# Optimization experiments

Hardware: AMD Instinct MI355X
Metric: run time of the kernel (lower is better)

Reference implementation:

```python
import jax, jax.numpy as jnp
import numpy as np

N = 50000
E = 800000
IN_C = 256
HID = 256
OUT_C = 128


def _glorot(key, fan_in, fan_out):
    lim = float(np.sqrt(6.0 / (fan_in + fan_out)))
    return jax.random.uniform(key, (fan_in, fan_out), jnp.float32, -lim, lim)


def setup_inputs() -> dict:
    key = jax.random.key(0)
    ks = jax.random.split(key, 10)
    x = jax.random.normal(ks[0], (N, IN_C), dtype=jnp.float32)
    edge_index = jax.random.randint(ks[1], (2, E), 0, N, dtype=jnp.int64)
    return {
        "x": x,
        "edge_index": edge_index,
        # layer 0 MLP: Linear(IN_C,HID)+ReLU+Linear(HID,HID)+ReLU
        "eps0": jnp.zeros((), jnp.float32),
        "W1_0": _glorot(ks[2], IN_C, HID),
        "b1_0": jnp.zeros((HID,), jnp.float32),
        "W2_0": _glorot(ks[3], HID, HID),
        "b2_0": jnp.zeros((HID,), jnp.float32),
        # layer 1 MLP: Linear(HID,HID)+ReLU+Linear(HID,OUT_C)
        "eps1": jnp.zeros((), jnp.float32),
        "W1_1": _glorot(ks[4], HID, HID),
        "b1_1": jnp.zeros((HID,), jnp.float32),
        "W2_1": _glorot(ks[5], HID, OUT_C),
        "b2_1": jnp.zeros((OUT_C,), jnp.float32),
    }


def _gin_layer(x, src, dst, eps, W1, b1, W2, b2, final_relu):
    # sum-aggregate messages x[src] into dst nodes
    agg = jax.ops.segment_sum(x[src], dst, num_segments=N)  # [N, d]
    h = (1.0 + eps) * x + agg
    h = jax.nn.relu(h @ W1 + b1)
    h = h @ W2 + b2
    return jax.nn.relu(h) if final_relu else h


def reference(x, edge_index, eps0, W1_0, b1_0, W2_0, b2_0, eps1, W1_1, b1_1, W2_1, b2_1):
    src, dst = edge_index[0], edge_index[1]
    h = _gin_layer(x, src, dst, eps0, W1_0, b1_0, W2_0, b2_0, final_relu=True)
    h = jax.nn.relu(h)  # model-level ReLU between layers
    h = _gin_layer(h, src, dst, eps1, W1_1, b1_1, W2_1, b2_1, final_relu=False)
    return jax.nn.log_softmax(h, axis=1)
```

## Files before the change

### kernel.cpp

```cpp
#include <hip/hip_runtime.h>
#include <hip/hip_bf16.h>

#define FDIM 256
#define OUTC 128
#define CAP  96

typedef float floatx4 __attribute__((ext_vector_type(4)));
typedef float floatx2 __attribute__((ext_vector_type(2)));
typedef __bf16 bf16x8 __attribute__((ext_vector_type(8)));

__device__ __forceinline__ unsigned short f2bf(float f) {
    union { float f; unsigned u; } v; v.f = f;
    unsigned r = v.u + 0x7FFF + ((v.u >> 16) & 1);
    return (unsigned short)(r >> 16);
}
__device__ __forceinline__ unsigned pack2(float a, float b) {
    return ((unsigned)f2bf(a)) | (((unsigned)f2bf(b)) << 16);
}
__device__ __forceinline__ void acc_row2(floatx2* a, uint4 v) {
    union { unsigned u; float f; } lo, hi;
    lo.u = v.x << 16; hi.u = v.x & 0xffff0000u; a[0] += (floatx2){lo.f, hi.f};
    lo.u = v.y << 16; hi.u = v.y & 0xffff0000u; a[1] += (floatx2){lo.f, hi.f};
    lo.u = v.z << 16; hi.u = v.z & 0xffff0000u; a[2] += (floatx2){lo.f, hi.f};
    lo.u = v.w << 16; hi.u = v.w & 0xffff0000u; a[3] += (floatx2){lo.f, hi.f};
}

__global__ __launch_bounds__(256)
void prep_kernel(const int* __restrict__ src, const int* __restrict__ dst,
                 int* __restrict__ cursor, int* __restrict__ esrc2, int E,
                 const float* __restrict__ x, unsigned short* __restrict__ xb, int total8,
                 const float* __restrict__ W1_0, const float* __restrict__ W2_0,
                 const float* __restrict__ W1_1, const float* __restrict__ W2_1,
                 unsigned short* __restrict__ w1f_0, unsigned short* __restrict__ w2f_0,
                 unsigned short* __restrict__ w1f_1, unsigned short* __restrict__ w2f_1) {
    int gid = blockIdx.x * 256 + threadIdx.x;
    if (gid < E) {
        int d = dst[gid];
        int pos = atomicAdd(&cursor[d], 1);
        if (pos < CAP) esrc2[d * CAP + pos] = src[gid];
        return;
    }
    gid -= E;
    if (gid < total8) {
        const float4* p = (const float4*)(x + (size_t)gid * 8);
        float4 a = p[0], b = p[1];
        uint4 o;
        o.x = pack2(a.x, a.y); o.y = pack2(a.z, a.w);
        o.z = pack2(b.x, b.y); o.w = pack2(b.z, b.w);
        *(uint4*)(xb + (size_t)gid * 8) = o;
        return;
    }
    gid -= total8;
    const int S = FDIM * FDIM;
    const float* W; unsigned short* WF; int local, J, Ncols;
    if (gid < S)          { W = W1_0; WF = w1f_0; local = gid;         J = 4; Ncols = FDIM; }
    else if (gid < 2 * S) { W = W2_0; WF = w2f_0; local = gid - S;     J = 4; Ncols = FDIM; }
    else if (gid < 3 * S) { W = W1_1; WF = w1f_1; local = gid - 2 * S; J = 4; Ncols = FDIM; }
    else if (gid < 3 * S + FDIM * OUTC)
                          { W = W2_1; WF = w2f_1; local = gid - 3 * S; J = 2; Ncols = OUTC; }
    else return;
    int e    = local & 7;
    int lane = (local >> 3) & 63;
    int l15  = lane & 15;
    int quad = lane >> 4;
    int rest = local >> 9;
    int j  = rest % J;  rest /= J;
    int kc = rest & 7;
    int g  = rest >> 3;
    int n = g * (16 * J) + j * 16 + l15;
    int k = kc * 32 + quad * 8 + e;
    WF[local] = f2bf(W[(size_t)k * Ncols + n]);
}

template<bool SELF_F32>
__global__ __launch_bounds__(256)
void gather2_kernel(const unsigned short* __restrict__ xb,
                    const float* __restrict__ xf,
                    const int* __restrict__ esrc2,
                    const int* __restrict__ cursor,
                    const float* __restrict__ epsp, unsigned short* __restrict__ out,
                    int N) {
    int node = (int)((blockIdx.x * blockDim.x + threadIdx.x) >> 6);
    int lane = threadIdx.x & 63;
    if (node >= N) return;
    int half = lane >> 5;
    int hl   = lane & 31;
    int beg = node * CAP;
    int cnt = cursor[node];
    if (cnt > CAP) cnt = CAP;

    floatx2 acc[4];
    acc[0] = (floatx2){0.f, 0.f}; acc[1] = (floatx2){0.f, 0.f};
    acc[2] = (floatx2){0.f, 0.f}; acc[3] = (floatx2){0.f, 0.f};

    int e = 0;
    for (; e + 16 <= cnt; e += 16) {
        int s[8];
        #pragma unroll
        for (int k = 0; k < 8; ++k) s[k] = esrc2[beg + e + 2 * k + half];
        uint4 v[8];
        #pragma unroll
        for (int k = 0; k < 8; ++k)
            v[k] = *(const uint4*)(xb + (size_t)s[k] * FDIM + hl * 8);
        #pragma unroll
        for (int k = 0; k < 8; ++k) acc_row2(acc, v[k]);
    }
    for (; e + 4 <= cnt; e += 4) {
        int s0 = esrc2[beg + e + half];
        int s1 = esrc2[beg + e + 2 + half];
        uint4 v0 = *(const uint4*)(xb + (size_t)s0 * FDIM + hl * 8);
        uint4 v1 = *(const uint4*)(xb + (size_t)s1 * FDIM + hl * 8);
        acc_row2(acc, v0);
        acc_row2(acc, v1);
    }
    if (e + 2 <= cnt) {
        int s0 = esrc2[beg + e + half];
        uint4 v0 = *(const uint4*)(xb + (size_t)s0 * FDIM + hl * 8);
        acc_row2(acc, v0);
        e += 2;
    }
    if (e < cnt && half == 0) {
        int s0 = esrc2[beg + e];
        uint4 v0 = *(const uint4*)(xb + (size_t)s0 * FDIM + hl * 8);
        acc_row2(acc, v0);
    }

    float a8[8];
    #pragma unroll
    for (int i = 0; i < 4; ++i) { a8[2 * i] = acc[i][0]; a8[2 * i + 1] = acc[i][1]; }
    #pragma unroll
    for (int i = 0; i < 8; ++i) a8[i] += __shfl_xor(a8[i], 32);

    if (half == 0) {
        float scale = 1.0f + *epsp;
        if (SELF_F32) {
            const float4* p = (const float4*)(xf + (size_t)node * FDIM + hl * 8);
            float4 a = p[0], b = p[1];
            a8[0] += scale * a.x; a8[1] += scale * a.y;
            a8[2] += scale * a.z; a8[3] += scale * a.w;
            a8[4] += scale * b.x; a8[5] += scale * b.y;
            a8[6] += scale * b.z; a8[7] += scale * b.w;
        } else {
            uint4 v = *(const uint4*)(xb + (size_t)node * FDIM + hl * 8);
            union { unsigned u; float f; } t;
            t.u = v.x << 16;         a8[0] += scale * t.f;
            t.u = v.x & 0xffff0000u; a8[1] += scale * t.f;
            t.u = v.y << 16;         a8[2] += scale * t.f;
            t.u = v.y & 0xffff0000u; a8[3] += scale * t.f;
            t.u = v.z << 16;         a8[4] += scale * t.f;
            t.u = v.z & 0xffff0000u; a8[5] += scale * t.f;
            t.u = v.w << 16;         a8[6] += scale * t.f;
            t.u = v.w & 0xffff0000u; a8[7] += scale * t.f;
        }
        uint4 o;
        o.x = pack2(a8[0], a8[1]);
        o.y = pack2(a8[2], a8[3]);
        o.z = pack2(a8[4], a8[5]);
        o.w = pack2(a8[6], a8[7]);
        *(uint4*)(out + (size_t)node * FDIM + hl * 8) = o;
    }
}

#define LDA 264

template<bool FINAL>
__global__ __launch_bounds__(256)
void mlp_fused_kernel(const unsigned short* __restrict__ A,
                      const unsigned short* __restrict__ W1F,
                      const float* __restrict__ b1,
                      const unsigned short* __restrict__ W2F,
                      const float* __restrict__ b2,
                      void* __restrict__ Out, int M) {
    __shared__ unsigned short As[64 * LDA];
    __shared__ float sred[64 * 4 * 2];

    int tid  = threadIdx.x;
    int wave = tid >> 6;
    int lane = tid & 63;
    int l15  = lane & 15;
    int quad = lane >> 4;
    int row0 = blockIdx.x * 64;

    #pragma unroll
    for (int i = 0; i < 8; ++i) {
        int idx = i * 256 + tid;
        int r = idx >> 5;
        int c = (idx & 31) * 8;
        uint4 v = make_uint4(0u, 0u, 0u, 0u);
        int gr = row0 + r;
        if (gr < M) v = *(const uint4*)(A + (size_t)gr * FDIM + c);
        *(uint4*)(As + r * LDA + c) = v;
    }
    __syncthreads();

    floatx4 zero = {0.f, 0.f, 0.f, 0.f};

    {
        floatx4 acc[4][4];
        #pragma unroll
        for (int i = 0; i < 4; ++i)
            #pragma unroll
            for (int j = 0; j < 4; ++j) acc[i][j] = zero;

        const unsigned short* Wb = W1F + (size_t)wave * 16384;
        bf16x8 bcur[4], bnxt[4];
        #pragma unroll
        for (int j = 0; j < 4; ++j)
            bcur[j] = *(const bf16x8*)(Wb + j * 512 + lane * 8);

        for (int kc = 0; kc < 8; ++kc) {
            const unsigned short* Wn = Wb + ((kc < 7) ? (kc + 1) : kc) * 2048;
            #pragma unroll
            for (int j = 0; j < 4; ++j)
                bnxt[j] = *(const bf16x8*)(Wn + j * 512 + lane * 8);
            bf16x8 af[4];
            int k = kc * 32;
            #pragma unroll
            for (int i = 0; i < 4; ++i)
                af[i] = *(const bf16x8*)(As + (i * 16 + l15) * LDA + k + quad * 8);
            #pragma unroll
            for (int i = 0; i < 4; ++i)
                #pragma unroll
                for (int j = 0; j < 4; ++j)
                    acc[i][j] = __builtin_amdgcn_mfma_f32_16x16x32_bf16(
                        af[i], bcur[j], acc[i][j], 0, 0, 0);
            #pragma unroll
            for (int j = 0; j < 4; ++j) bcur[j] = bnxt[j];
        }

        __syncthreads();

        #pragma unroll
        for (int j = 0; j < 4; ++j) {
            int col = wave * 64 + j * 16 + l15;
            float bv = b1[col];
            #pragma unroll
            for (int i = 0; i < 4; ++i) {
                #pragma unroll
                for (int r = 0; r < 4; ++r) {
                    float v = fmaxf(acc[i][j][r] + bv, 0.f);
                    As[(i * 16 + quad * 4 + r) * LDA + col] = f2bf(v);
                }
            }
        }
    }
    __syncthreads();

    if (!FINAL) {
        floatx4 acc[4][4];
        #pragma unroll
        for (int i = 0; i < 4; ++i)
            #pragma unroll
            for (int j = 0; j < 4; ++j) acc[i][j] = zero;

        const unsigned short* Wb = W2F + (size_t)wave * 16384;
        bf16x8 bcur[4], bnxt[4];
        #pragma unroll
        for (int j = 0; j < 4; ++j)
            bcur[j] = *(const bf16x8*)(Wb + j * 512 + lane * 8);

        for (int kc = 0; kc < 8; ++kc) {
            const unsigned short* Wn = Wb + ((kc < 7) ? (kc + 1) : kc) * 2048;
            #pragma unroll
            for (int j = 0; j < 4; ++j)
                bnxt[j] = *(const bf16x8*)(Wn + j * 512 + lane * 8);
            bf16x8 af[4];
            int k = kc * 32;
            #pragma unroll
            for (int i = 0; i < 4; ++i)
                af[i] = *(const bf16x8*)(As + (i * 16 + l15) * LDA + k + quad * 8);
            #pragma unroll
            for (int i = 0; i < 4; ++i)
                #pragma unroll
                for (int j = 0; j < 4; ++j)
                    acc[i][j] = __builtin_amdgcn_mfma_f32_16x16x32_bf16(
                        af[i], bcur[j], acc[i][j], 0, 0, 0);
            #pragma unroll
            for (int j = 0; j < 4; ++j) bcur[j] = bnxt[j];
        }

        unsigned short* O = (unsigned short*)Out;
        #pragma unroll
        for (int j = 0; j < 4; ++j) {
            int col = wave * 64 + j * 16 + l15;
            float bv = b2[col];
            #pragma unroll
            for (int i = 0; i < 4; ++i) {
                #pragma unroll
                for (int r = 0; r < 4; ++r) {
                    int grow = row0 + i * 16 + quad * 4 + r;
                    if (grow < M) {
                        float v = fmaxf(acc[i][j][r] + bv, 0.f);
                        O[(size_t)grow * FDIM + col] = f2bf(v);
                    }
                }
            }
        }
    } else {
        floatx4 acc[4][2];
        #pragma unroll
        for (int i = 0; i < 4; ++i)
            #pragma unroll
            for (int j = 0; j < 2; ++j) acc[i][j] = zero;

        const unsigned short* Wb = W2F + (size_t)wave * 8192;
        bf16x8 bcur[2], bnxt[2];
        #pragma unroll
        for (int j = 0; j < 2; ++j)
            bcur[j] = *(const bf16x8*)(Wb + j * 512 + lane * 8);

        for (int kc = 0; kc < 8; ++kc) {
            const unsigned short* Wn = Wb + ((kc < 7) ? (kc + 1) : kc) * 1024;
            #pragma unroll
            for (int j = 0; j < 2; ++j)
                bnxt[j] = *(const bf16x8*)(Wn + j * 512 + lane * 8);
            bf16x8 af[4];
            int k = kc * 32;
            #pragma unroll
            for (int i = 0; i < 4; ++i)
                af[i] = *(const bf16x8*)(As + (i * 16 + l15) * LDA + k + quad * 8);
            #pragma unroll
            for (int i = 0; i < 4; ++i)
                #pragma unroll
                for (int j = 0; j < 2; ++j)
                    acc[i][j] = __builtin_amdgcn_mfma_f32_16x16x32_bf16(
                        af[i], bcur[j], acc[i][j], 0, 0, 0);
            #pragma unroll
            for (int j = 0; j < 2; ++j) bcur[j] = bnxt[j];
        }

        #pragma unroll
        for (int j = 0; j < 2; ++j) {
            float bv = b2[wave * 32 + j * 16 + l15];
            #pragma unroll
            for (int i = 0; i < 4; ++i)
                #pragma unroll
                for (int r = 0; r < 4; ++r) acc[i][j][r] += bv;
        }

        float* smax = sred;
        float* ssum = sred + 256;

        #pragma unroll
        for (int i = 0; i < 4; ++i) {
            #pragma unroll
            for (int r = 0; r < 4; ++r) {
                float m = fmaxf(acc[i][0][r], acc[i][1][r]);
                #pragma unroll
                for (int off = 1; off < 16; off <<= 1) m = fmaxf(m, __shfl_xor(m, off));
                int row = i * 16 + quad * 4 + r;
                if (l15 == 0) smax[row * 4 + wave] = m;
            }
        }
        __syncthreads();

        float Mloc[4][4];
        #pragma unroll
        for (int i = 0; i < 4; ++i) {
            #pragma unroll
            for (int r = 0; r < 4; ++r) {
                int row = i * 16 + quad * 4 + r;
                float Mr = fmaxf(fmaxf(smax[row * 4 + 0], smax[row * 4 + 1]),
                                 fmaxf(smax[row * 4 + 2], smax[row * 4 + 3]));
                Mloc[i][r] = Mr;
                float s = __expf(acc[i][0][r] - Mr) + __expf(acc[i][1][r] - Mr);
                #pragma unroll
                for (int off = 1; off < 16; off <<= 1) s += __shfl_xor(s, off);
                if (l15 == 0) ssum[row * 4 + wave] = s;
            }
        }
        __syncthreads();

        float* O = (float*)Out;
        #pragma unroll
        for (int i = 0; i < 4; ++i) {
            #pragma unroll
            for (int r = 0; r < 4; ++r) {
                int row = i * 16 + quad * 4 + r;
                int grow = row0 + row;
                if (grow < M) {
                    float lse = Mloc[i][r] +
                        __logf(ssum[row * 4 + 0] + ssum[row * 4 + 1] +
                               ssum[row * 4 + 2] + ssum[row * 4 + 3]);
                    #pragma unroll
                    for (int j = 0; j < 2; ++j) {
                        int col = wave * 32 + j * 16 + l15;
                        O[(size_t)grow * OUTC + col] = acc[i][j][r] - lse;
                    }
                }
            }
        }
    }
}

extern "C" void kernel_launch(void* const* d_in, const int* in_sizes, int n_in,
                              void* d_out, int out_size, void* d_ws, size_t ws_size,
                              hipStream_t stream) {
    const float* x    = (const float*)d_in[0];
    const int*   ei   = (const int*)d_in[1];
    const float* eps0 = (const float*)d_in[2];
    const float* W1_0 = (const float*)d_in[3];
    const float* b1_0 = (const float*)d_in[4];
    const float* W2_0 = (const float*)d_in[5];
    const float* b2_0 = (const float*)d_in[6];
    const float* eps1 = (const float*)d_in[7];
    const float* W1_1 = (const float*)d_in[8];
    const float* b1_1 = (const float*)d_in[9];
    const float* W2_1 = (const float*)d_in[10];
    const float* b2_1 = (const float*)d_in[11];
    float* out = (float*)d_out;

    const int N = in_sizes[0] / FDIM;
    const int E = in_sizes[1] / 2;
    const int* src = ei;
    const int* dst = ei + E;

    size_t buf_elems = (size_t)N * FDIM;
    unsigned short* agg = (unsigned short*)d_ws;
    unsigned short* h2  = agg + buf_elems;
    unsigned short* xb  = h2 + buf_elems;
    unsigned short* w1f_0 = xb + buf_elems;
    unsigned short* w2f_0 = w1f_0 + FDIM * FDIM;
    unsigned short* w1f_1 = w2f_0 + FDIM * FDIM;
    unsigned short* w2f_1 = w1f_1 + FDIM * FDIM;
    int* cursor = (int*)(w2f_1 + FDIM * OUTC);
    int* esrc2  = cursor + N;

    int gather_blocks = (N + 3) / 4;
    int mlp_blocks = (N + 63) / 64;
    int total8 = (int)(buf_elems / 8);
    int wtot = 3 * FDIM * FDIM + FDIM * OUTC;
    int prep_threads = E + total8 + wtot;

    hipMemsetAsync(cursor, 0, (size_t)N * sizeof(int), stream);
    prep_kernel<<<(prep_threads + 255) / 256, 256, 0, stream>>>(
        src, dst, cursor, esrc2, E, x, xb, total8,
        W1_0, W2_0, W1_1, W2_1, w1f_0, w2f_0, w1f_1, w2f_1);

    gather2_kernel<true><<<gather_blocks, 256, 0, stream>>>(
        xb, x, esrc2, cursor, eps0, agg, N);
    mlp_fused_kernel<false><<<mlp_blocks, 256, 0, stream>>>(
        agg, w1f_0, b1_0, w2f_0, b2_0, h2, N);

    gather2_kernel<false><<<gather_blocks, 256, 0, stream>>>(
        h2, nullptr, esrc2, cursor, eps1, agg, N);
    mlp_fused_kernel<true><<<mlp_blocks, 256, 0, stream>>>(
        agg, w1f_1, b1_1, w2f_1, b2_1, out, N);
}
```

Baseline: 349.8 us.

## Fuse neighbor gather-aggregation into the MLP kernel via shared-memory staging

Replaces the separate gather kernel and MLP kernel with one kernel per layer. Each block's waves aggregate their 16 nodes' neighbor rows directly into shared memory before the fused two-layer GEMM. This removes the intermediate aggregated buffer's global write and read and two launches. A zero row is appended so partially filled edge chunks read padding instead of branching. The risk is reduced memory-level parallelism for the irregular gather, since fewer waves, bounded by LDS use, now do serial per-node gathers.

```diff
diff --git a/kernel.cpp b/kernel.cpp
--- a/kernel.cpp
+++ b/kernel.cpp
@@ -1,9 +1,9 @@
 #include <hip/hip_runtime.h>
-#include <hip/hip_bf16.h>
 
 #define FDIM 256
 #define OUTC 128
 #define CAP  96
+#define LDA 264
 
 typedef float floatx4 __attribute__((ext_vector_type(4)));
 typedef float floatx2 __attribute__((ext_vector_type(2)));
@@ -32,7 +32,8 @@
                  const float* __restrict__ W1_0, const float* __restrict__ W2_0,
                  const float* __restrict__ W1_1, const float* __restrict__ W2_1,
                  unsigned short* __restrict__ w1f_0, unsigned short* __restrict__ w2f_0,
-                 unsigned short* __restrict__ w1f_1, unsigned short* __restrict__ w2f_1) {
+                 unsigned short* __restrict__ w1f_1, unsigned short* __restrict__ w2f_1,
+                 unsigned short* __restrict__ xzrow, unsigned short* __restrict__ hzrow) {
     int gid = blockIdx.x * 256 + threadIdx.x;
     if (gid < E) {
         int d = dst[gid];
@@ -52,125 +53,45 @@
     }
     gid -= total8;
     const int S = FDIM * FDIM;
-    const float* W; unsigned short* WF; int local, J, Ncols;
-    if (gid < S)          { W = W1_0; WF = w1f_0; local = gid;         J = 4; Ncols = FDIM; }
-    else if (gid < 2 * S) { W = W2_0; WF = w2f_0; local = gid - S;     J = 4; Ncols = FDIM; }
-    else if (gid < 3 * S) { W = W1_1; WF = w1f_1; local = gid - 2 * S; J = 4; Ncols = FDIM; }
-    else if (gid < 3 * S + FDIM * OUTC)
-                          { W = W2_1; WF = w2f_1; local = gid - 3 * S; J = 2; Ncols = OUTC; }
-    else return;
-    int e    = local & 7;
-    int lane = (local >> 3) & 63;
-    int l15  = lane & 15;
-    int quad = lane >> 4;
-    int rest = local >> 9;
-    int j  = rest % J;  rest /= J;
-    int kc = rest & 7;
-    int g  = rest >> 3;
-    int n = g * (16 * J) + j * 16 + l15;
-    int k = kc * 32 + quad * 8 + e;
-    WF[local] = f2bf(W[(size_t)k * Ncols + n]);
-}
-
-template<bool SELF_F32>
+    const int wtot = 3 * S + FDIM * OUTC;
+    if (gid < wtot) {
+        const float* W; unsigned short* WF; int local, J, Ncols;
+        if (gid < S)          { W = W1_0; WF = w1f_0; local = gid;         J = 4; Ncols = FDIM; }
+        else if (gid < 2 * S) { W = W2_0; WF = w2f_0; local = gid - S;     J = 4; Ncols = FDIM; }
+        else if (gid < 3 * S) { W = W1_1; WF = w1f_1; local = gid - 2 * S; J = 4; Ncols = FDIM; }
+        else                  { W = W2_1; WF = w2f_1; local = gid - 3 * S; J = 2; Ncols = OUTC; }
+        int e    = local & 7;
+        int lane = (local >> 3) & 63;
+        int l15  = lane & 15;
+        int quad = lane >> 4;
+        int rest = local >> 9;
+        int j  = rest % J;  rest /= J;
+        int kc = rest & 7;
+        int g  = rest >> 3;
+        int n = g * (16 * J) + j * 16 + l15;
+        int k = kc * 32 + quad * 8 + e;
+        WF[local] = f2bf(W[(size_t)k * Ncols + n]);
+        return;
+    }
+    gid -= wtot;
+    uint4 z = make_uint4(0u, 0u, 0u, 0u);
+    if (gid < 32) { *(uint4*)(xzrow + gid * 8) = z; return; }
+    gid -= 32;
+    if (gid < 32) { *(uint4*)(hzrow + gid * 8) = z; }
+}
+
+template<bool SELF_F32, bool FINAL>
 __global__ __launch_bounds__(256)
-void gather2_kernel(const unsigned short* __restrict__ xb,
+void gin_mlp_kernel(const unsigned short* __restrict__ xb,
                     const float* __restrict__ xf,
                     const int* __restrict__ esrc2,
                     const int* __restrict__ cursor,
-                    const float* __restrict__ epsp, unsigned short* __restrict__ out,
-                    int N) {
-    int node = (int)((blockIdx.x * blockDim.x + threadIdx.x) >> 6);
-    int lane = threadIdx.x & 63;
-    if (node >= N) return;
-    int half = lane >> 5;
-    int hl   = lane & 31;
-    int beg = node * CAP;
-    int cnt = cursor[node];
-    if (cnt > CAP) cnt = CAP;
-
-    floatx2 acc[4];
-    acc[0] = (floatx2){0.f, 0.f}; acc[1] = (floatx2){0.f, 0.f};
-    acc[2] = (floatx2){0.f, 0.f}; acc[3] = (floatx2){0.f, 0.f};
-
-    int e = 0;
-    for (; e + 16 <= cnt; e += 16) {
-        int s[8];
-        #pragma unroll
-        for (int k = 0; k < 8; ++k) s[k] = esrc2[beg + e + 2 * k + half];
-        uint4 v[8];
-        #pragma unroll
-        for (int k = 0; k < 8; ++k)
-            v[k] = *(const uint4*)(xb + (size_t)s[k] * FDIM + hl * 8);
-        #pragma unroll
-        for (int k = 0; k < 8; ++k) acc_row2(acc, v[k]);
-    }
-    for (; e + 4 <= cnt; e += 4) {
-        int s0 = esrc2[beg + e + half];
-        int s1 = esrc2[beg + e + 2 + half];
-        uint4 v0 = *(const uint4*)(xb + (size_t)s0 * FDIM + hl * 8);
-        uint4 v1 = *(const uint4*)(xb + (size_t)s1 * FDIM + hl * 8);
-        acc_row2(acc, v0);
-        acc_row2(acc, v1);
-    }
-    if (e + 2 <= cnt) {
-        int s0 = esrc2[beg + e + half];
-        uint4 v0 = *(const uint4*)(xb + (size_t)s0 * FDIM + hl * 8);
-        acc_row2(acc, v0);
-        e += 2;
-    }
-    if (e < cnt && half == 0) {
-        int s0 = esrc2[beg + e];
-        uint4 v0 = *(const uint4*)(xb + (size_t)s0 * FDIM + hl * 8);
-        acc_row2(acc, v0);
-    }
-
-    float a8[8];
-    #pragma unroll
-    for (int i = 0; i < 4; ++i) { a8[2 * i] = acc[i][0]; a8[2 * i + 1] = acc[i][1]; }
-    #pragma unroll
-    for (int i = 0; i < 8; ++i) a8[i] += __shfl_xor(a8[i], 32);
-
-    if (half == 0) {
-        float scale = 1.0f + *epsp;
-        if (SELF_F32) {
-            const float4* p = (const float4*)(xf + (size_t)node * FDIM + hl * 8);
-            float4 a = p[0], b = p[1];
-            a8[0] += scale * a.x; a8[1] += scale * a.y;
-            a8[2] += scale * a.z; a8[3] += scale * a.w;
-            a8[4] += scale * b.x; a8[5] += scale * b.y;
-            a8[6] += scale * b.z; a8[7] += scale * b.w;
-        } else {
-            uint4 v = *(const uint4*)(xb + (size_t)node * FDIM + hl * 8);
-            union { unsigned u; float f; } t;
-            t.u = v.x << 16;         a8[0] += scale * t.f;
-            t.u = v.x & 0xffff0000u; a8[1] += scale * t.f;
-            t.u = v.y << 16;         a8[2] += scale * t.f;
-            t.u = v.y & 0xffff0000u; a8[3] += scale * t.f;
-            t.u = v.z << 16;         a8[4] += scale * t.f;
-            t.u = v.z & 0xffff0000u; a8[5] += scale * t.f;
-            t.u = v.w << 16;         a8[6] += scale * t.f;
-            t.u = v.w & 0xffff0000u; a8[7] += scale * t.f;
-        }
-        uint4 o;
-        o.x = pack2(a8[0], a8[1]);
-        o.y = pack2(a8[2], a8[3]);
-        o.z = pack2(a8[4], a8[5]);
-        o.w = pack2(a8[6], a8[7]);
-        *(uint4*)(out + (size_t)node * FDIM + hl * 8) = o;
-    }
-}
-
-#define LDA 264
-
-template<bool FINAL>
-__global__ __launch_bounds__(256)
-void mlp_fused_kernel(const unsigned short* __restrict__ A,
-                      const unsigned short* __restrict__ W1F,
-                      const float* __restrict__ b1,
-                      const unsigned short* __restrict__ W2F,
-                      const float* __restrict__ b2,
-                      void* __restrict__ Out, int M) {
+                    const float* __restrict__ epsp,
+                    const unsigned short* __restrict__ W1F,
+                    const float* __restrict__ b1,
+                    const unsigned short* __restrict__ W2F,
+                    const float* __restrict__ b2,
+                    void* __restrict__ Out, int N) {
     __shared__ unsigned short As[64 * LDA];
     __shared__ float sred[64 * 4 * 2];
 
@@ -179,17 +100,72 @@
     int lane = tid & 63;
     int l15  = lane & 15;
     int quad = lane >> 4;
+    int half = lane >> 5;
+    int hl   = lane & 31;
     int row0 = blockIdx.x * 64;
 
-    #pragma unroll
-    for (int i = 0; i < 8; ++i) {
-        int idx = i * 256 + tid;
-        int r = idx >> 5;
-        int c = (idx & 31) * 8;
-        uint4 v = make_uint4(0u, 0u, 0u, 0u);
-        int gr = row0 + r;
-        if (gr < M) v = *(const uint4*)(A + (size_t)gr * FDIM + c);
-        *(uint4*)(As + r * LDA + c) = v;
+    float scale = 1.0f + *epsp;
+
+    for (int i = 0; i < 16; ++i) {
+        int lrow = wave * 16 + i;
+        int node = row0 + lrow;
+        floatx2 acc[4];
+        acc[0] = (floatx2){0.f, 0.f}; acc[1] = (floatx2){0.f, 0.f};
+        acc[2] = (floatx2){0.f, 0.f}; acc[3] = (floatx2){0.f, 0.f};
+        bool valid = node < N;
+        int cnt = 0;
+        if (valid) { cnt = cursor[node]; if (cnt > CAP) cnt = CAP; }
+        int beg = node * CAP;
+        for (int e = 0; e < cnt; e += 16) {
+            int s[8];
+            #pragma unroll
+            for (int k = 0; k < 8; ++k) {
+                int slot = e + 2 * k + half;
+                int si = esrc2[beg + slot];
+                s[k] = (slot < cnt) ? si : N;
+            }
+            uint4 v[8];
+            #pragma unroll
+            for (int k = 0; k < 8; ++k)
+                v[k] = *(const uint4*)(xb + (size_t)s[k] * FDIM + hl * 8);
+            #pragma unroll
+            for (int k = 0; k < 8; ++k) acc_row2(acc, v[k]);
+        }
+        float a8[8];
+        #pragma unroll
+        for (int j = 0; j < 4; ++j) { a8[2 * j] = acc[j][0]; a8[2 * j + 1] = acc[j][1]; }
+        #pragma unroll
+        for (int j = 0; j < 8; ++j) a8[j] += __shfl_xor(a8[j], 32);
+
+        if (half == 0) {
+            if (valid) {
+                if (SELF_F32) {
+                    const float4* p = (const float4*)(xf + (size_t)node * FDIM + hl * 8);
+                    float4 a = p[0], b = p[1];
+                    a8[0] += scale * a.x; a8[1] += scale * a.y;
+                    a8[2] += scale * a.z; a8[3] += scale * a.w;
+                    a8[4] += scale * b.x; a8[5] += scale * b.y;
+                    a8[6] += scale * b.z; a8[7] += scale * b.w;
+                } else {
+                    uint4 v = *(const uint4*)(xb + (size_t)node * FDIM + hl * 8);
+                    union { unsigned u; float f; } t;
+                    t.u = v.x << 16;         a8[0] += scale * t.f;
+                    t.u = v.x & 0xffff0000u; a8[1] += scale * t.f;
+                    t.u = v.y << 16;         a8[2] += scale * t.f;
+                    t.u = v.y & 0xffff0000u; a8[3] += scale * t.f;
+                    t.u = v.z << 16;         a8[4] += scale * t.f;
+                    t.u = v.z & 0xffff0000u; a8[5] += scale * t.f;
+                    t.u = v.w << 16;         a8[6] += scale * t.f;
+                    t.u = v.w & 0xffff0000u; a8[7] += scale * t.f;
+                }
+            }
+            uint4 o;
+            o.x = pack2(a8[0], a8[1]);
+            o.y = pack2(a8[2], a8[3]);
+            o.z = pack2(a8[4], a8[5]);
+            o.w = pack2(a8[6], a8[7]);
+            *(uint4*)(As + lrow * LDA + hl * 8) = o;
+        }
     }
     __syncthreads();
 
@@ -289,7 +265,7 @@
                 #pragma unroll
                 for (int r = 0; r < 4; ++r) {
                     int grow = row0 + i * 16 + quad * 4 + r;
-                    if (grow < M) {
+                    if (grow < N) {
                         float v = fmaxf(acc[i][j][r] + bv, 0.f);
                         O[(size_t)grow * FDIM + col] = f2bf(v);
                     }
@@ -378,7 +354,7 @@
             for (int r = 0; r < 4; ++r) {
                 int row = i * 16 + quad * 4 + r;
                 int grow = row0 + row;
-                if (grow < M) {
+                if (grow < N) {
                     float lse = Mloc[i][r] +
                         __logf(ssum[row * 4 + 0] + ssum[row * 4 + 1] +
                                ssum[row * 4 + 2] + ssum[row * 4 + 3]);
@@ -415,35 +391,30 @@
     const int* src = ei;
     const int* dst = ei + E;
 
-    size_t buf_elems = (size_t)N * FDIM;
-    unsigned short* agg = (unsigned short*)d_ws;
-    unsigned short* h2  = agg + buf_elems;
-    unsigned short* xb  = h2 + buf_elems;
-    unsigned short* w1f_0 = xb + buf_elems;
+    size_t row_elems = (size_t)(N + 1) * FDIM;
+    unsigned short* h2  = (unsigned short*)d_ws;
+    unsigned short* xb  = h2 + row_elems;
+    unsigned short* w1f_0 = xb + row_elems;
     unsigned short* w2f_0 = w1f_0 + FDIM * FDIM;
     unsigned short* w1f_1 = w2f_0 + FDIM * FDIM;
     unsigned short* w2f_1 = w1f_1 + FDIM * FDIM;
     int* cursor = (int*)(w2f_1 + FDIM * OUTC);
     int* esrc2  = cursor + N;
 
-    int gather_blocks = (N + 3) / 4;
     int mlp_blocks = (N + 63) / 64;
-    int total8 = (int)(buf_elems / 8);
+    int total8 = (int)((size_t)N * FDIM / 8);
     int wtot = 3 * FDIM * FDIM + FDIM * OUTC;
-    int prep_threads = E + total8 + wtot;
+    int prep_threads = E + total8 + wtot + 64;
 
     hipMemsetAsync(cursor, 0, (size_t)N * sizeof(int), stream);
     prep_kernel<<<(prep_threads + 255) / 256, 256, 0, stream>>>(
         src, dst, cursor, esrc2, E, x, xb, total8,
-        W1_0, W2_0, W1_1, W2_1, w1f_0, w2f_0, w1f_1, w2f_1);
-
-    gather2_kernel<true><<<gather_blocks, 256, 0, stream>>>(
-        xb, x, esrc2, cursor, eps0, agg, N);
-    mlp_fused_kernel<false><<<mlp_blocks, 256, 0, stream>>>(
-        agg, w1f_0, b1_0, w2f_0, b2_0, h2, N);
-
-    gather2_kernel<false><<<gather_blocks, 256, 0, stream>>>(
-        h2, nullptr, esrc2, cursor, eps1, agg, N);
-    mlp_fused_kernel<true><<<mlp_blocks, 256, 0, stream>>>(
-        agg, w1f_1, b1_1, w2f_1, b2_1, out, N);
-}
+        W1_0, W2_0, W1_1, W2_1, w1f_0, w2f_0, w1f_1, w2f_1,
+        xb + (size_t)N * FDIM, h2 + (size_t)N * FDIM);
+
+    gin_mlp_kernel<true, false><<<mlp_blocks, 256, 0, stream>>>(
+        xb, x, esrc2, cursor, eps0, w1f_0, b1_0, w2f_0, b2_0, h2, N);
+
+    gin_mlp_kernel<false, true><<<mlp_blocks, 256, 0, stream>>>(
+        h2, nullptr, esrc2, cursor, eps1, w1f_1, b1_1, w2f_1, b2_1, out, N);
+}
```

Measured after the change: 371.3 us. 1.06x slower.

## Fuse all stages into one persistent cooperative kernel with grid syncs

Applied to the files above, without the earlier changes.

Replaces the memset plus five separate launches with a single persistent cooperative kernel. Each stage (cursor clear, prep, gather, MLP, gather, MLP) is a grid-stride loop separated by grid.sync, and the grid is sized from occupancy. The goal is to remove per-launch overhead and inter-kernel gaps. In exchange it limits resident blocks (launch_bounds 256,4 may force register spills in the MLP), adds grid-wide barrier cost, and loses the latency hiding that comes from oversubscribing blocks in the gather. A fallback multi-kernel path covers the case where the cooperative launch fails.

```diff
diff --git a/kernel.cpp b/kernel.cpp
--- a/kernel.cpp
+++ b/kernel.cpp
@@ -1,9 +1,12 @@
 #include <hip/hip_runtime.h>
-#include <hip/hip_bf16.h>
+#include <hip/hip_cooperative_groups.h>
+
+namespace cg = cooperative_groups;
 
 #define FDIM 256
 #define OUTC 128
 #define CAP  96
+#define LDA 264
 
 typedef float floatx4 __attribute__((ext_vector_type(4)));
 typedef float floatx2 __attribute__((ext_vector_type(2)));
@@ -25,40 +28,43 @@
     lo.u = v.w << 16; hi.u = v.w & 0xffff0000u; a[3] += (floatx2){lo.f, hi.f};
 }
 
-__global__ __launch_bounds__(256)
-void prep_kernel(const int* __restrict__ src, const int* __restrict__ dst,
-                 int* __restrict__ cursor, int* __restrict__ esrc2, int E,
-                 const float* __restrict__ x, unsigned short* __restrict__ xb, int total8,
-                 const float* __restrict__ W1_0, const float* __restrict__ W2_0,
-                 const float* __restrict__ W1_1, const float* __restrict__ W2_1,
-                 unsigned short* __restrict__ w1f_0, unsigned short* __restrict__ w2f_0,
-                 unsigned short* __restrict__ w1f_1, unsigned short* __restrict__ w2f_1) {
-    int gid = blockIdx.x * 256 + threadIdx.x;
-    if (gid < E) {
-        int d = dst[gid];
-        int pos = atomicAdd(&cursor[d], 1);
-        if (pos < CAP) esrc2[d * CAP + pos] = src[gid];
+struct UberParams {
+    const int* src; const int* dst;
+    int* cursor; int* esrc2;
+    int E; int N; int total8;
+    const float* x; unsigned short* xb;
+    const float* W1_0; const float* W2_0; const float* W1_1; const float* W2_1;
+    unsigned short* w1f_0; unsigned short* w2f_0; unsigned short* w1f_1; unsigned short* w2f_1;
+    const float* b1_0; const float* b2_0; const float* b1_1; const float* b2_1;
+    const float* eps0; const float* eps1;
+    unsigned short* agg; unsigned short* h2;
+    float* out;
+};
+
+__device__ __forceinline__ void prep_work(int gid, const UberParams& p) {
+    if (gid < p.E) {
+        int d = p.dst[gid];
+        int pos = atomicAdd(&p.cursor[d], 1);
+        if (pos < CAP) p.esrc2[d * CAP + pos] = p.src[gid];
         return;
     }
-    gid -= E;
-    if (gid < total8) {
-        const float4* p = (const float4*)(x + (size_t)gid * 8);
-        float4 a = p[0], b = p[1];
+    gid -= p.E;
+    if (gid < p.total8) {
+        const float4* q = (const float4*)(p.x + (size_t)gid * 8);
+        float4 a = q[0], b = q[1];
         uint4 o;
         o.x = pack2(a.x, a.y); o.y = pack2(a.z, a.w);
         o.z = pack2(b.x, b.y); o.w = pack2(b.z, b.w);
-        *(uint4*)(xb + (size_t)gid * 8) = o;
+        *(uint4*)(p.xb + (size_t)gid * 8) = o;
         return;
     }
-    gid -= total8;
+    gid -= p.total8;
     const int S = FDIM * FDIM;
     const float* W; unsigned short* WF; int local, J, Ncols;
-    if (gid < S)          { W = W1_0; WF = w1f_0; local = gid;         J = 4; Ncols = FDIM; }
-    else if (gid < 2 * S) { W = W2_0; WF = w2f_0; local = gid - S;     J = 4; Ncols = FDIM; }
-    else if (gid < 3 * S) { W = W1_1; WF = w1f_1; local = gid - 2 * S; J = 4; Ncols = FDIM; }
-    else if (gid < 3 * S + FDIM * OUTC)
-                          { W = W2_1; WF = w2f_1; local = gid - 3 * S; J = 2; Ncols = OUTC; }
-    else return;
+    if (gid < S)          { W = p.W1_0; WF = p.w1f_0; local = gid;         J = 4; Ncols = FDIM; }
+    else if (gid < 2 * S) { W = p.W2_0; WF = p.w2f_0; local = gid - S;     J = 4; Ncols = FDIM; }
+    else if (gid < 3 * S) { W = p.W1_1; WF = p.w1f_1; local = gid - 2 * S; J = 4; Ncols = FDIM; }
+    else                  { W = p.W2_1; WF = p.w2f_1; local = gid - 3 * S; J = 2; Ncols = OUTC; }
     int e    = local & 7;
     int lane = (local >> 3) & 63;
     int l15  = lane & 15;
@@ -73,16 +79,11 @@
 }
 
 template<bool SELF_F32>
-__global__ __launch_bounds__(256)
-void gather2_kernel(const unsigned short* __restrict__ xb,
-                    const float* __restrict__ xf,
-                    const int* __restrict__ esrc2,
-                    const int* __restrict__ cursor,
-                    const float* __restrict__ epsp, unsigned short* __restrict__ out,
-                    int N) {
-    int node = (int)((blockIdx.x * blockDim.x + threadIdx.x) >> 6);
-    int lane = threadIdx.x & 63;
-    if (node >= N) return;
+__device__ __forceinline__ void gather_node(
+        int node, const unsigned short* __restrict__ xbuf,
+        const float* __restrict__ xf,
+        const int* __restrict__ esrc2, const int* __restrict__ cursor,
+        float scale, unsigned short* __restrict__ outb, int lane) {
     int half = lane >> 5;
     int hl   = lane & 31;
     int beg = node * CAP;
@@ -101,27 +102,27 @@
         uint4 v[8];
         #pragma unroll
         for (int k = 0; k < 8; ++k)
-            v[k] = *(const uint4*)(xb + (size_t)s[k] * FDIM + hl * 8);
+            v[k] = *(const uint4*)(xbuf + (size_t)s[k] * FDIM + hl * 8);
         #pragma unroll
         for (int k = 0; k < 8; ++k) acc_row2(acc, v[k]);
     }
     for (; e + 4 <= cnt; e += 4) {
         int s0 = esrc2[beg + e + half];
         int s1 = esrc2[beg + e + 2 + half];
-        uint4 v0 = *(const uint4*)(xb + (size_t)s0 * FDIM + hl * 8);
-        uint4 v1 = *(const uint4*)(xb + (size_t)s1 * FDIM + hl * 8);
+        uint4 v0 = *(const uint4*)(xbuf + (size_t)s0 * FDIM + hl * 8);
+        uint4 v1 = *(const uint4*)(xbuf + (size_t)s1 * FDIM + hl * 8);
         acc_row2(acc, v0);
         acc_row2(acc, v1);
     }
     if (e + 2 <= cnt) {
         int s0 = esrc2[beg + e + half];
-        uint4 v0 = *(const uint4*)(xb + (size_t)s0 * FDIM + hl * 8);
+        uint4 v0 = *(const uint4*)(xbuf + (size_t)s0 * FDIM + hl * 8);
         acc_row2(acc, v0);
         e += 2;
     }
     if (e < cnt && half == 0) {
         int s0 = esrc2[beg + e];
-        uint4 v0 = *(const uint4*)(xb + (size_t)s0 * FDIM + hl * 8);
+        uint4 v0 = *(const uint4*)(xbuf + (size_t)s0 * FDIM + hl * 8);
         acc_row2(acc, v0);
     }
 
@@ -132,16 +133,15 @@
     for (int i = 0; i < 8; ++i) a8[i] += __shfl_xor(a8[i], 32);
 
     if (half == 0) {
-        float scale = 1.0f + *epsp;
         if (SELF_F32) {
-            const float4* p = (const float4*)(xf + (size_t)node * FDIM + hl * 8);
-            float4 a = p[0], b = p[1];
+            const float4* q = (const float4*)(xf + (size_t)node * FDIM + hl * 8);
+            float4 a = q[0], b = q[1];
             a8[0] += scale * a.x; a8[1] += scale * a.y;
             a8[2] += scale * a.z; a8[3] += scale * a.w;
             a8[4] += scale * b.x; a8[5] += scale * b.y;
             a8[6] += scale * b.z; a8[7] += scale * b.w;
         } else {
-            uint4 v = *(const uint4*)(xb + (size_t)node * FDIM + hl * 8);
+            uint4 v = *(const uint4*)(xbuf + (size_t)node * FDIM + hl * 8);
             union { unsigned u; float f; } t;
             t.u = v.x << 16;         a8[0] += scale * t.f;
             t.u = v.x & 0xffff0000u; a8[1] += scale * t.f;
@@ -157,29 +157,24 @@
         o.y = pack2(a8[2], a8[3]);
         o.z = pack2(a8[4], a8[5]);
         o.w = pack2(a8[6], a8[7]);
-        *(uint4*)(out + (size_t)node * FDIM + hl * 8) = o;
-    }
-}
-
-#define LDA 264
+        *(uint4*)(outb + (size_t)node * FDIM + hl * 8) = o;
+    }
+}
 
 template<bool FINAL>
-__global__ __launch_bounds__(256)
-void mlp_fused_kernel(const unsigned short* __restrict__ A,
-                      const unsigned short* __restrict__ W1F,
-                      const float* __restrict__ b1,
-                      const unsigned short* __restrict__ W2F,
-                      const float* __restrict__ b2,
-                      void* __restrict__ Out, int M) {
-    __shared__ unsigned short As[64 * LDA];
-    __shared__ float sred[64 * 4 * 2];
-
-    int tid  = threadIdx.x;
+__device__ __forceinline__ void mlp_tile(
+        int t, const unsigned short* __restrict__ A,
+        const unsigned short* __restrict__ W1F, const float* __restrict__ b1,
+        const unsigned short* __restrict__ W2F, const float* __restrict__ b2,
+        void* __restrict__ Out, int N,
+        unsigned short* As, float* sred, int tid) {
     int wave = tid >> 6;
     int lane = tid & 63;
     int l15  = lane & 15;
     int quad = lane >> 4;
-    int row0 = blockIdx.x * 64;
+    int row0 = t * 64;
+
+    __syncthreads();
 
     #pragma unroll
     for (int i = 0; i < 8; ++i) {
@@ -188,7 +183,7 @@
         int c = (idx & 31) * 8;
         uint4 v = make_uint4(0u, 0u, 0u, 0u);
         int gr = row0 + r;
-        if (gr < M) v = *(const uint4*)(A + (size_t)gr * FDIM + c);
+        if (gr < N) v = *(const uint4*)(A + (size_t)gr * FDIM + c);
         *(uint4*)(As + r * LDA + c) = v;
     }
     __syncthreads();
@@ -289,7 +284,7 @@
                 #pragma unroll
                 for (int r = 0; r < 4; ++r) {
                     int grow = row0 + i * 16 + quad * 4 + r;
-                    if (grow < M) {
+                    if (grow < N) {
                         float v = fmaxf(acc[i][j][r] + bv, 0.f);
                         O[(size_t)grow * FDIM + col] = f2bf(v);
                     }
@@ -378,7 +373,7 @@
             for (int r = 0; r < 4; ++r) {
                 int row = i * 16 + quad * 4 + r;
                 int grow = row0 + row;
-                if (grow < M) {
+                if (grow < N) {
                     float lse = Mloc[i][r] +
                         __logf(ssum[row * 4 + 0] + ssum[row * 4 + 1] +
                                ssum[row * 4 + 2] + ssum[row * 4 + 3]);
@@ -391,6 +386,86 @@
             }
         }
     }
+}
+
+__global__ __launch_bounds__(256, 4)
+void uber_kernel(UberParams p) {
+    __shared__ unsigned short As[64 * LDA];
+    __shared__ float sred[64 * 4 * 2];
+
+    cg::grid_group grid = cg::this_grid();
+    int tid = threadIdx.x;
+    int nthreads = gridDim.x * 256;
+    int gid0 = blockIdx.x * 256 + tid;
+
+    for (int i = gid0; i < p.N; i += nthreads) p.cursor[i] = 0;
+    __threadfence();
+    grid.sync();
+
+    int prep_items = p.E + p.total8 + 3 * FDIM * FDIM + FDIM * OUTC;
+    for (int it = gid0; it < prep_items; it += nthreads) prep_work(it, p);
+    __threadfence();
+    grid.sync();
+
+    {
+        int wid = blockIdx.x * 4 + (tid >> 6);
+        int nw  = gridDim.x * 4;
+        float scale = 1.0f + *p.eps0;
+        for (int node = wid; node < p.N; node += nw)
+            gather_node<true>(node, p.xb, p.x, p.esrc2, p.cursor, scale, p.agg, tid & 63);
+    }
+    __threadfence();
+    grid.sync();
+
+    {
+        int ntiles = (p.N + 63) / 64;
+        for (int t = blockIdx.x; t < ntiles; t += gridDim.x)
+            mlp_tile<false>(t, p.agg, p.w1f_0, p.b1_0, p.w2f_0, p.b2_0, p.h2, p.N, As, sred, tid);
+    }
+    __threadfence();
+    grid.sync();
+
+    {
+        int wid = blockIdx.x * 4 + (tid >> 6);
+        int nw  = gridDim.x * 4;
+        float scale = 1.0f + *p.eps1;
+        for (int node = wid; node < p.N; node += nw)
+            gather_node<false>(node, p.h2, nullptr, p.esrc2, p.cursor, scale, p.agg, tid & 63);
+    }
+    __threadfence();
+    grid.sync();
+
+    {
+        int ntiles = (p.N + 63) / 64;
+        for (int t = blockIdx.x; t < ntiles; t += gridDim.x)
+            mlp_tile<true>(t, p.agg, p.w1f_1, p.b1_1, p.w2f_1, p.b2_1, p.out, p.N, As, sred, tid);
+    }
+}
+
+__global__ __launch_bounds__(256)
+void prep_kernel_f(UberParams p) {
+    int gid = blockIdx.x * 256 + threadIdx.x;
+    int items = p.E + p.total8 + 3 * FDIM * FDIM + FDIM * OUTC;
+    if (gid < items) prep_work(gid, p);
+}
+
+__global__ __launch_bounds__(256)
+void gather_kernel_f(UberParams p, int layer) {
+    int wid = (int)((blockIdx.x * blockDim.x + threadIdx.x) >> 6);
+    if (wid >= p.N) return;
+    if (layer == 0)
+        gather_node<true>(wid, p.xb, p.x, p.esrc2, p.cursor, 1.0f + *p.eps0, p.agg, threadIdx.x & 63);
+    else
+        gather_node<false>(wid, p.h2, nullptr, p.esrc2, p.cursor, 1.0f + *p.eps1, p.agg, threadIdx.x & 63);
+}
+
+template<bool FINAL>
+__global__ __launch_bounds__(256)
+void mlp_kernel_f(const unsigned short* A, const unsigned short* W1F, const float* b1,
+                  const unsigned short* W2F, const float* b2, void* Out, int N) {
+    __shared__ unsigned short As[64 * LDA];
+    __shared__ float sred[64 * 4 * 2];
+    mlp_tile<FINAL>(blockIdx.x, A, W1F, b1, W2F, b2, Out, N, As, sred, threadIdx.x);
 }
 
 extern "C" void kernel_launch(void* const* d_in, const int* in_sizes, int n_in,
@@ -412,8 +487,6 @@
 
     const int N = in_sizes[0] / FDIM;
     const int E = in_sizes[1] / 2;
-    const int* src = ei;
-    const int* dst = ei + E;
 
     size_t buf_elems = (size_t)N * FDIM;
     unsigned short* agg = (unsigned short*)d_ws;
@@ -426,24 +499,46 @@
     int* cursor = (int*)(w2f_1 + FDIM * OUTC);
     int* esrc2  = cursor + N;
 
-    int gather_blocks = (N + 3) / 4;
-    int mlp_blocks = (N + 63) / 64;
-    int total8 = (int)(buf_elems / 8);
-    int wtot = 3 * FDIM * FDIM + FDIM * OUTC;
-    int prep_threads = E + total8 + wtot;
-
-    hipMemsetAsync(cursor, 0, (size_t)N * sizeof(int), stream);
-    prep_kernel<<<(prep_threads + 255) / 256, 256, 0, stream>>>(
-        src, dst, cursor, esrc2, E, x, xb, total8,
-        W1_0, W2_0, W1_1, W2_1, w1f_0, w2f_0, w1f_1, w2f_1);
-
-    gather2_kernel<true><<<gather_blocks, 256, 0, stream>>>(
-        xb, x, esrc2, cursor, eps0, agg, N);
-    mlp_fused_kernel<false><<<mlp_blocks, 256, 0, stream>>>(
-        agg, w1f_0, b1_0, w2f_0, b2_0, h2, N);
-
-    gather2_kernel<false><<<gather_blocks, 256, 0, stream>>>(
-        h2, nullptr, esrc2, cursor, eps1, agg, N);
-    mlp_fused_kernel<true><<<mlp_blocks, 256, 0, stream>>>(
-        agg, w1f_1, b1_1, w2f_1, b2_1, out, N);
-}
+    UberParams p;
+    p.src = ei; p.dst = ei + E;
+    p.cursor = cursor; p.esrc2 = esrc2;
+    p.E = E; p.N = N; p.total8 = (int)(buf_elems / 8);
+    p.x = x; p.xb = xb;
+    p.W1_0 = W1_0; p.W2_0 = W2_0; p.W1_1 = W1_1; p.W2_1 = W2_1;
+    p.w1f_0 = w1f_0; p.w2f_0 = w2f_0; p.w1f_1 = w1f_1; p.w2f_1 = w2f_1;
+    p.b1_0 = b1_0; p.b2_0 = b2_0; p.b1_1 = b1_1; p.b2_1 = b2_1;
+    p.eps0 = eps0; p.eps1 = eps1;
+    p.agg = agg; p.h2 = h2; p.out = out;
+
+    static int grid_blocks = 0;
+    if (grid_blocks == 0) {
+        int blocksPerCU = 0;
+        hipError_t e1 = hipOccupancyMaxActiveBlocksPerMultiprocessor(
+            &blocksPerCU, uber_kernel, 256, 0);
+        int numCU = 0, dev = 0;
+        hipGetDevice(&dev);
+        hipDeviceGetAttribute(&numCU, hipDeviceAttributeMultiprocessorCount, dev);
+        if (e1 != hipSuccess || blocksPerCU < 1) blocksPerCU = 1;
+        if (numCU <= 0) numCU = 256;
+        grid_blocks = blocksPerCU * numCU;
+        if (grid_blocks < 256) grid_blocks = 256;
+    }
+
+    void* args[] = { (void*)&p };
+    hipError_t rc = hipLaunchCooperativeKernel(
+        (const void*)uber_kernel, dim3(grid_blocks), dim3(256), args, 0, stream);
+
+    if (rc != hipSuccess) {
+        int gather_blocks = (N + 3) / 4;
+        int mlp_blocks = (N + 63) / 64;
+        int prep_items = E + p.total8 + 3 * FDIM * FDIM + FDIM * OUTC;
+        hipMemsetAsync(cursor, 0, (size_t)N * sizeof(int), stream);
+        prep_kernel_f<<<(prep_items + 255) / 256, 256, 0, stream>>>(p);
+        gather_kernel_f<<<gather_blocks, 256, 0, stream>>>(p, 0);
+        mlp_kernel_f<false><<<mlp_blocks, 256, 0, stream>>>(
+            agg, w1f_0, b1_0, w2f_0, b2_0, h2, N);
+        gather_kernel_f<<<gather_blocks, 256, 0, stream>>>(p, 1);
+        mlp_kernel_f<true><<<mlp_blocks, 256, 0, stream>>>(
+            agg, w1f_1, b1_1, w2f_1, b2_1, out, N);
+    }
+}
```

Result: slower. 1.114 ms (+218.3%).

## Rework gather to full-wave rows, pad atomic cursors, masked tail loop

Applied to the files above, without the earlier changes.

The gather kernel now has each 64-lane wave read a whole 256-element bf16 row (8 bytes per lane) for 16 neighbours at a time, where before each half-wave handled one edge and the halves were combined with a cross-half shuffle. The tail is handled by one masked 16-wide batch that reloads a valid index in place of the separate 4/2/1 remainder loops. Per-node atomic cursors are padded to 64-byte strides to cut contention and false sharing during CSR bucketing. In exchange, each load is narrower, the cursor memset is 16x larger, and the tail batch issues redundant loads.

```diff
diff --git a/kernel.cpp b/kernel.cpp
--- a/kernel.cpp
+++ b/kernel.cpp
@@ -1,12 +1,12 @@
 #include <hip/hip_runtime.h>
-#include <hip/hip_bf16.h>
 
 #define FDIM 256
 #define OUTC 128
 #define CAP  96
+#define CURS 16
+#define LDA 264
 
 typedef float floatx4 __attribute__((ext_vector_type(4)));
-typedef float floatx2 __attribute__((ext_vector_type(2)));
 typedef __bf16 bf16x8 __attribute__((ext_vector_type(8)));
 
 __device__ __forceinline__ unsigned short f2bf(float f) {
@@ -17,12 +17,10 @@
 __device__ __forceinline__ unsigned pack2(float a, float b) {
     return ((unsigned)f2bf(a)) | (((unsigned)f2bf(b)) << 16);
 }
-__device__ __forceinline__ void acc_row2(floatx2* a, uint4 v) {
+__device__ __forceinline__ void add4(float* a, uint2 v) {
     union { unsigned u; float f; } lo, hi;
-    lo.u = v.x << 16; hi.u = v.x & 0xffff0000u; a[0] += (floatx2){lo.f, hi.f};
-    lo.u = v.y << 16; hi.u = v.y & 0xffff0000u; a[1] += (floatx2){lo.f, hi.f};
-    lo.u = v.z << 16; hi.u = v.z & 0xffff0000u; a[2] += (floatx2){lo.f, hi.f};
-    lo.u = v.w << 16; hi.u = v.w & 0xffff0000u; a[3] += (floatx2){lo.f, hi.f};
+    lo.u = v.x << 16; hi.u = v.x & 0xffff0000u; a[0] += lo.f; a[1] += hi.f;
+    lo.u = v.y << 16; hi.u = v.y & 0xffff0000u; a[2] += lo.f; a[3] += hi.f;
 }
 
 __global__ __launch_bounds__(256)
@@ -36,7 +34,7 @@
     int gid = blockIdx.x * 256 + threadIdx.x;
     if (gid < E) {
         int d = dst[gid];
-        int pos = atomicAdd(&cursor[d], 1);
+        int pos = atomicAdd(&cursor[d * CURS], 1);
         if (pos < CAP) esrc2[d * CAP + pos] = src[gid];
         return;
     }
@@ -80,88 +78,61 @@
                     const int* __restrict__ cursor,
                     const float* __restrict__ epsp, unsigned short* __restrict__ out,
                     int N) {
-    int node = (int)((blockIdx.x * blockDim.x + threadIdx.x) >> 6);
+    int node = __builtin_amdgcn_readfirstlane(
+        (int)((blockIdx.x * blockDim.x + threadIdx.x) >> 6));
     int lane = threadIdx.x & 63;
     if (node >= N) return;
-    int half = lane >> 5;
-    int hl   = lane & 31;
+    int col = lane * 4;
     int beg = node * CAP;
-    int cnt = cursor[node];
+    int cnt = cursor[node * CURS];
     if (cnt > CAP) cnt = CAP;
 
-    floatx2 acc[4];
-    acc[0] = (floatx2){0.f, 0.f}; acc[1] = (floatx2){0.f, 0.f};
-    acc[2] = (floatx2){0.f, 0.f}; acc[3] = (floatx2){0.f, 0.f};
+    float a4[4] = {0.f, 0.f, 0.f, 0.f};
 
     int e = 0;
     for (; e + 16 <= cnt; e += 16) {
-        int s[8];
-        #pragma unroll
-        for (int k = 0; k < 8; ++k) s[k] = esrc2[beg + e + 2 * k + half];
-        uint4 v[8];
-        #pragma unroll
-        for (int k = 0; k < 8; ++k)
-            v[k] = *(const uint4*)(xb + (size_t)s[k] * FDIM + hl * 8);
-        #pragma unroll
-        for (int k = 0; k < 8; ++k) acc_row2(acc, v[k]);
-    }
-    for (; e + 4 <= cnt; e += 4) {
-        int s0 = esrc2[beg + e + half];
-        int s1 = esrc2[beg + e + 2 + half];
-        uint4 v0 = *(const uint4*)(xb + (size_t)s0 * FDIM + hl * 8);
-        uint4 v1 = *(const uint4*)(xb + (size_t)s1 * FDIM + hl * 8);
-        acc_row2(acc, v0);
-        acc_row2(acc, v1);
-    }
-    if (e + 2 <= cnt) {
-        int s0 = esrc2[beg + e + half];
-        uint4 v0 = *(const uint4*)(xb + (size_t)s0 * FDIM + hl * 8);
-        acc_row2(acc, v0);
-        e += 2;
-    }
-    if (e < cnt && half == 0) {
-        int s0 = esrc2[beg + e];
-        uint4 v0 = *(const uint4*)(xb + (size_t)s0 * FDIM + hl * 8);
-        acc_row2(acc, v0);
-    }
-
-    float a8[8];
-    #pragma unroll
-    for (int i = 0; i < 4; ++i) { a8[2 * i] = acc[i][0]; a8[2 * i + 1] = acc[i][1]; }
-    #pragma unroll
-    for (int i = 0; i < 8; ++i) a8[i] += __shfl_xor(a8[i], 32);
-
-    if (half == 0) {
-        float scale = 1.0f + *epsp;
-        if (SELF_F32) {
-            const float4* p = (const float4*)(xf + (size_t)node * FDIM + hl * 8);
-            float4 a = p[0], b = p[1];
-            a8[0] += scale * a.x; a8[1] += scale * a.y;
-            a8[2] += scale * a.z; a8[3] += scale * a.w;
-            a8[4] += scale * b.x; a8[5] += scale * b.y;
-            a8[6] += scale * b.z; a8[7] += scale * b.w;
-        } else {
-            uint4 v = *(const uint4*)(xb + (size_t)node * FDIM + hl * 8);
-            union { unsigned u; float f; } t;
-            t.u = v.x << 16;         a8[0] += scale * t.f;
-            t.u = v.x & 0xffff0000u; a8[1] += scale * t.f;
-            t.u = v.y << 16;         a8[2] += scale * t.f;
-            t.u = v.y & 0xffff0000u; a8[3] += scale * t.f;
-            t.u = v.z << 16;         a8[4] += scale * t.f;
-            t.u = v.z & 0xffff0000u; a8[5] += scale * t.f;
-            t.u = v.w << 16;         a8[6] += scale * t.f;
-            t.u = v.w & 0xffff0000u; a8[7] += scale * t.f;
-        }
-        uint4 o;
-        o.x = pack2(a8[0], a8[1]);
-        o.y = pack2(a8[2], a8[3]);
-        o.z = pack2(a8[4], a8[5]);
-        o.w = pack2(a8[6], a8[7]);
-        *(uint4*)(out + (size_t)node * FDIM + hl * 8) = o;
-    }
-}
-
-#define LDA 264
+        int s[16];
+        #pragma unroll
+        for (int k = 0; k < 16; ++k) s[k] = esrc2[beg + e + k];
+        uint2 v[16];
+        #pragma unroll
+        for (int k = 0; k < 16; ++k)
+            v[k] = *(const uint2*)(xb + (size_t)s[k] * FDIM + col);
+        #pragma unroll
+        for (int k = 0; k < 16; ++k) add4(a4, v[k]);
+    }
+    int rem = cnt - e;
+    if (rem > 0) {
+        int s[16];
+        #pragma unroll
+        for (int k = 0; k < 16; ++k) s[k] = esrc2[beg + e + ((k < rem) ? k : 0)];
+        uint2 v[16];
+        #pragma unroll
+        for (int k = 0; k < 16; ++k)
+            v[k] = *(const uint2*)(xb + (size_t)s[k] * FDIM + col);
+        #pragma unroll
+        for (int k = 0; k < 16; ++k)
+            if (k < rem) add4(a4, v[k]);
+    }
+
+    float scale = 1.0f + *epsp;
+    if (SELF_F32) {
+        float4 sv = *(const float4*)(xf + (size_t)node * FDIM + col);
+        a4[0] += scale * sv.x; a4[1] += scale * sv.y;
+        a4[2] += scale * sv.z; a4[3] += scale * sv.w;
+    } else {
+        uint2 sv = *(const uint2*)(xb + (size_t)node * FDIM + col);
+        union { unsigned u; float f; } t;
+        t.u = sv.x << 16;         a4[0] += scale * t.f;
+        t.u = sv.x & 0xffff0000u; a4[1] += scale * t.f;
+        t.u = sv.y << 16;         a4[2] += scale * t.f;
+        t.u = sv.y & 0xffff0000u; a4[3] += scale * t.f;
+    }
+    uint2 o;
+    o.x = pack2(a4[0], a4[1]);
+    o.y = pack2(a4[2], a4[3]);
+    *(uint2*)(out + (size_t)node * FDIM + col) = o;
+}
 
 template<bool FINAL>
 __global__ __launch_bounds__(256)
@@ -424,7 +395,7 @@
     unsigned short* w1f_1 = w2f_0 + FDIM * FDIM;
     unsigned short* w2f_1 = w1f_1 + FDIM * FDIM;
     int* cursor = (int*)(w2f_1 + FDIM * OUTC);
-    int* esrc2  = cursor + N;
+    int* esrc2  = cursor + (size_t)N * CURS;
 
     int gather_blocks = (N + 3) / 4;
     int mlp_blocks = (N + 63) / 64;
@@ -432,7 +403,7 @@
     int wtot = 3 * FDIM * FDIM + FDIM * OUTC;
     int prep_threads = E + total8 + wtot;
 
-    hipMemsetAsync(cursor, 0, (size_t)N * sizeof(int), stream);
+    hipMemsetAsync(cursor, 0, (size_t)N * CURS * sizeof(int), stream);
     prep_kernel<<<(prep_threads + 255) / 256, 256, 0, stream>>>(
         src, dst, cursor, esrc2, E, x, xb, total8,
         W1_0, W2_0, W1_1, W2_1, w1f_0, w2f_0, w1f_1, w2f_1);
```

New measurement: 346.4 us. About the same (-1.0%).
